# Performance work log

Measured on AMD Instinct MI355X. Metric: run time of the kernel, lower is better.

Reference implementation:

```python
import jax, jax.numpy as jnp
import numpy as np

DIMS = (8, 8, 16, 16)   # 4D lattice, prod = 16384 sites
ND = len(DIMS)
N_IN = 4
N_OUT = 4
NC = 3
KERNEL_SIZE = 2
DILATION = 0
INIT_W = 1.0

W_IN = 2 * N_IN + 1                                  # 9
T_W = 2 * (N_IN * (KERNEL_SIZE - 1) * ND) + 1        # 33


def cconj(w):
    # swap matrix indices (axes 3,4) and negate imaginary part (last axis)
    wT = jnp.swapaxes(w, 3, 4)
    return wT * jnp.array([1.0, -1.0], dtype=w.dtype)


def complex_einsum(pattern, a, b, conj_a=1, conj_b=1):
    aR, aI = a[..., 0], conj_a * a[..., 1]
    bR, bI = b[..., 0], conj_b * b[..., 1]
    cR = jnp.einsum(pattern, aR, bR) - jnp.einsum(pattern, aI, bI)
    cI = jnp.einsum(pattern, aR, bI) + jnp.einsum(pattern, aI, bR)
    return jnp.stack((cR, cI), axis=-1)


def shift(a, axis, orientation):
    # dim 1 is flattened lattice; unflatten, roll along lattice axis, re-flatten
    o_s = a.shape
    n_s = (o_s[0],) + DIMS + o_s[2:]
    return jnp.roll(a.reshape(n_s), orientation, axis=axis + 1).reshape(o_s)


def transport(u, w, axis):
    # positive-orientation gauge transport: U w(x+mu) U^dagger
    ws = shift(w, axis, -1)
    ua = u[:, :, axis]                                 # [b, x, nc, nc, 2]
    wt = complex_einsum('bxij,bxwjk->bxwik', ua, ws)
    wt = complex_einsum('bxwij,bxkj->bxwik', wt, ua, conj_b=-1)
    return wt


def setup_inputs() -> dict:
    key = jax.random.key(0)
    k1, k2 = jax.random.split(key)
    n_sites = int(np.prod(DIMS))
    x = jax.random.normal(k1, (1, n_sites, ND + N_IN, NC, NC, 2), dtype=jnp.float32)
    std = INIT_W * np.sqrt(1.0 / (W_IN * T_W))
    weight = jax.random.normal(k2, (N_OUT, W_IN, T_W), dtype=jnp.float32) * std
    return {"x": x, "weight": weight}


def reference(x, weight):
    u, w = x[:, :, :ND], x[:, :, ND:]
    transported = []
    for axis in range(ND):
        wt = w
        for d in range(1, KERNEL_SIZE):
            for _ in range(DILATION + 1):
                wt = transport(u, wt, axis)
            transported.append(wt)
    t_w = jnp.concatenate(transported, axis=2)          # [b, x, n_in*(K-1)*ND, nc, nc, 2]

    w_full = jnp.concatenate([w, cconj(w)], axis=2)
    t_w_full = jnp.concatenate([t_w, cconj(t_w)], axis=2)

    # unit element channel
    unit = jnp.stack((jnp.eye(NC, dtype=x.dtype), jnp.zeros((NC, NC), dtype=x.dtype)), axis=-1)
    b, n_sites = x.shape[0], x.shape[1]
    unit_t = jnp.broadcast_to(unit[None, None, None], (b, n_sites, 1, NC, NC, 2))
    w_full = jnp.concatenate([w_full, unit_t], axis=2)       # [b, x, 9, nc, nc, 2]
    t_w_full = jnp.concatenate([t_w_full, unit_t], axis=2)   # [b, x, 33, nc, nc, 2]

    # bilinear gauge-covariant products, then weight contraction
    ww = complex_einsum('bxvij,bxwjk->bxvwik', w_full, t_w_full)  # [b, x, 9, 33, nc, nc, 2]
    w_out = jnp.einsum('uvw,bxvwijc->bxuijc', weight, ww)         # [b, x, n_out, nc, nc, 2]

    return jnp.concatenate([u, w_out], axis=2)
```

## Files before the change

### kernel.cpp

```cpp
#include <hip/hip_runtime.h>
#include <stdint.h>


#define SPB 16
#define TPB 256
#define NSITES 16384
#define TS2_SITE 146
#define NWGT 1188

__device__ __forceinline__ float2 pk_fma(float2 a, float2 b, float2 c){
    return make_float2(fmaf(a.x, b.x, c.x), fmaf(a.y, b.y, c.y));
}
__device__ __forceinline__ float2 spl(float s){ return make_float2(s, s); }
__device__ __forceinline__ float2 pn(float s){ return make_float2(s, -s); }
__device__ __forceinline__ float2 np(float s){ return make_float2(-s, s); }
__device__ __forceinline__ float2 swp(float2 a){ return make_float2(a.y, a.x); }

__device__ __forceinline__ int neigh(int s, int a){
    if (a == 3) return (s & ~15)        | ((s + 1)    & 15);
    if (a == 2) return (s & ~(15 << 4)) | ((s + 16)   & (15 << 4));
    if (a == 1) return (s & ~(7 << 8))  | ((s + 256)  & (7 << 8));
    return              (s & ~(7 << 11))| ((s + 2048) & (7 << 11));
}

__global__ __launch_bounds__(TPB, 1)
void gcm_fused(const float* __restrict__ xp,
               const float* __restrict__ wgt,
               float* __restrict__ outp)
{
    __shared__ float2 lt[SPB * TS2_SITE];
    __shared__ float wsm[NWGT];
    const float2* x2 = (const float2*)xp;
    float2* o2 = (float2*)outp;

    const int tid = threadIdx.x;
    const int g   = tid & 3;
    const int u   = (tid >> 2) & 3;
    const int sl  = tid >> 4;
    const int s   = blockIdx.x * SPB + sl;

    for (int idx = tid; idx < NWGT; idx += TPB) wsm[idx] = wgt[idx];

    {
        const int a = u, i = g;
        float2 uc[9], wc[9];
        {
            const float2* up = x2 + (s * 8 + a) * 9;
            #pragma unroll
            for (int e = 0; e < 9; e++) uc[e] = up[e];
        }
        const int sn = neigh(s, a);
        {
            const float2* wp = x2 + (sn * 8 + 4 + i) * 9;
            #pragma unroll
            for (int e = 0; e < 9; e++) wc[e] = wp[e];
        }
        float2 t1[9];
        #pragma unroll
        for (int r = 0; r < 3; r++){
            #pragma unroll
            for (int k = 0; k < 3; k++){
                float2 acc = make_float2(0.f, 0.f);
                #pragma unroll
                for (int j = 0; j < 3; j++){
                    float2 a_ = uc[r*3+j], b_ = wc[j*3+k];
                    acc = pk_fma(spl(a_.x), b_, acc);
                    acc = pk_fma(np(a_.y), swp(b_), acc);
                }
                t1[r*3+k] = acc;
            }
        }
        float2* dst = &lt[sl * TS2_SITE + (a * 4 + i) * 9];
        #pragma unroll
        for (int r = 0; r < 3; r++){
            #pragma unroll
            for (int k = 0; k < 3; k++){
                float2 acc = make_float2(0.f, 0.f);
                #pragma unroll
                for (int j = 0; j < 3; j++){
                    float2 a_ = t1[r*3+j], b_ = uc[k*3+j];
                    acc = pk_fma(pn(a_.x), b_, acc);
                    acc = pk_fma(spl(a_.y), swp(b_), acc);
                }
                dst[r*3+k] = acc;
            }
        }
    }
    __syncthreads();

    if (g == 1){
        const float2* src = x2 + (s * 8 + u) * 9;
        float2* dst = o2 + (s * 8 + u) * 9;
        #pragma unroll
        for (int e = 0; e < 9; e++) dst[e] = src[e];
    }

    float2 wc[4][9];
    #pragma unroll
    for (int v = 0; v < 4; v++){
        const float2* wp = x2 + (s * 8 + 4 + v) * 9;
        #pragma unroll
        for (int e = 0; e < 9; e++) wc[v][e] = wp[e];
    }

    float2 cc[9];
    #pragma unroll
    for (int e = 0; e < 9; e++) cc[e] = make_float2(0.f, 0.f);

    const float* wu = wsm + u * 297;

    {
        #pragma unroll
        for (int v = 0; v < 4; v++){
            float c1 = (v == g) ? wu[v * 33 + 32]       : 0.f;
            float c2 = (v == g) ? wu[(4 + v) * 33 + 32] : 0.f;
            #pragma unroll
            for (int i = 0; i < 3; i++){
                #pragma unroll
                for (int j = 0; j < 3; j++){
                    const int e = i*3+j, eT = j*3+i;
                    cc[e] = pk_fma(spl(c1), wc[v][e],  cc[e]);
                    cc[e] = pk_fma(pn(c2),  wc[v][eT], cc[e]);
                }
            }
        }
        if (g == 0){
            float c8 = wu[8 * 33 + 32];
            cc[0].x += c8; cc[4].x += c8; cc[8].x += c8;
        }
    }

    const float2* tbase = &lt[sl * TS2_SITE];
    #pragma unroll
    for (int k = 0; k < 4; k++){
        const int w16 = g * 4 + k;
        float2 tc[9];
        {
            const float2* tp = tbase + w16 * 9;
            #pragma unroll
            for (int e = 0; e < 9; e++) tc[e] = tp[e];
        }

        {
            float cv[9];
            #pragma unroll
            for (int v = 0; v < 9; v++) cv[v] = wu[v * 33 + w16];
            #pragma unroll
            for (int i = 0; i < 3; i++){
                float2 nrow[3];
                #pragma unroll
                for (int j = 0; j < 3; j++){
                    const int e = i*3+j, eT = j*3+i;
                    float2 n = (i == j) ? make_float2(cv[8], 0.f) : make_float2(0.f, 0.f);
                    #pragma unroll
                    for (int v = 0; v < 4; v++){
                        n = pk_fma(spl(cv[v]),   wc[v][e],  n);
                        n = pk_fma(pn(cv[4+v]),  wc[v][eT], n);
                    }
                    nrow[j] = n;
                }
                #pragma unroll
                for (int kk = 0; kk < 3; kk++){
                    float2 acc = cc[i*3+kk];
                    #pragma unroll
                    for (int j = 0; j < 3; j++){
                        float2 b_ = tc[j*3+kk];
                        acc = pk_fma(spl(nrow[j].x), b_,      acc);
                        acc = pk_fma(np(nrow[j].y),  swp(b_), acc);
                    }
                    cc[i*3+kk] = acc;
                }
            }
        }

        {
            float cv[9];
            #pragma unroll
            for (int v = 0; v < 9; v++) cv[v] = wu[v * 33 + 16 + w16];
            #pragma unroll
            for (int i = 0; i < 3; i++){
                float2 nrow[3];
                #pragma unroll
                for (int j = 0; j < 3; j++){
                    const int e = i*3+j, eT = j*3+i;
                    float2 n = (i == j) ? make_float2(cv[8], 0.f) : make_float2(0.f, 0.f);
                    #pragma unroll
                    for (int v = 0; v < 4; v++){
                        n = pk_fma(spl(cv[v]),   wc[v][e],  n);
                        n = pk_fma(pn(cv[4+v]),  wc[v][eT], n);
                    }
                    nrow[j] = n;
                }
                #pragma unroll
                for (int kk = 0; kk < 3; kk++){
                    float2 acc = cc[i*3+kk];
                    #pragma unroll
                    for (int j = 0; j < 3; j++){
                        float2 b_ = tc[kk*3+j];
                        acc = pk_fma(pn(nrow[j].x),  b_,      acc);
                        acc = pk_fma(spl(nrow[j].y), swp(b_), acc);
                    }
                    cc[i*3+kk] = acc;
                }
            }
        }
    }

    #pragma unroll
    for (int e = 0; e < 9; e++){
        cc[e].x += __shfl_xor(cc[e].x, 1);
        cc[e].x += __shfl_xor(cc[e].x, 2);
        cc[e].y += __shfl_xor(cc[e].y, 1);
        cc[e].y += __shfl_xor(cc[e].y, 2);
    }
    if (g == 0){
        float2* dst = o2 + (s * 8 + 4 + u) * 9;
        #pragma unroll
        for (int e = 0; e < 9; e++) dst[e] = cc[e];
    }
}

extern "C" void kernel_launch(void* const* d_in, const int* in_sizes, int n_in,
                              void* d_out, int out_size, void* d_ws, size_t ws_size,
                              hipStream_t stream)
{
    const float* x = (const float*)d_in[0];
    const float* w = (const float*)d_in[1];
    float* out = (float*)d_out;
    dim3 grid(NSITES / SPB);
    dim3 block(TPB);
    hipLaunchKernelGGL(gcm_fused, grid, block, 0, stream, x, w, out);
}
```

Measured before the change: 88.93 us.

## Reassociate bilinear contraction: per-input weighted sums of transported fields

Each thread now owns one input channel g. It first accumulates two weighted linear combinations M1 and M2 of all 16 transported matrices (and their conjugates) from shared memory, then does just two 3x3 complex matmuls with w_g and its conjugate at the end. Before, each thread rebuilt weighted sums of all 4 w matrices for each of its own transported matrices and then did a matmul for each. The reordering cuts the 3x3 matmul count and drops the per-thread copy of all four w matrices, lowering register pressure. Launch bounds are raised to 2 blocks per SM to allow more occupancy. In exchange, each thread now reads all 16 transported matrices from LDS instead of 4, which raises LDS traffic.

```diff
diff --git a/kernel.cpp b/kernel.cpp
--- a/kernel.cpp
+++ b/kernel.cpp
@@ -23,7 +23,7 @@
     return              (s & ~(7 << 11))| ((s + 2048) & (7 << 11));
 }
 
-__global__ __launch_bounds__(TPB, 1)
+__global__ __launch_bounds__(TPB, 2)
 void gcm_fused(const float* __restrict__ xp,
                const float* __restrict__ wgt,
                float* __restrict__ outp)
@@ -95,114 +95,104 @@
         for (int e = 0; e < 9; e++) dst[e] = src[e];
     }
 
-    float2 wc[4][9];
-    #pragma unroll
-    for (int v = 0; v < 4; v++){
-        const float2* wp = x2 + (s * 8 + 4 + v) * 9;
-        #pragma unroll
-        for (int e = 0; e < 9; e++) wc[v][e] = wp[e];
-    }
-
-    float2 cc[9];
-    #pragma unroll
-    for (int e = 0; e < 9; e++) cc[e] = make_float2(0.f, 0.f);
-
-    const float* wu = wsm + u * 297;
-
+    float2 wg[9];
     {
-        #pragma unroll
-        for (int v = 0; v < 4; v++){
-            float c1 = (v == g) ? wu[v * 33 + 32]       : 0.f;
-            float c2 = (v == g) ? wu[(4 + v) * 33 + 32] : 0.f;
-            #pragma unroll
-            for (int i = 0; i < 3; i++){
-                #pragma unroll
-                for (int j = 0; j < 3; j++){
-                    const int e = i*3+j, eT = j*3+i;
-                    cc[e] = pk_fma(spl(c1), wc[v][e],  cc[e]);
-                    cc[e] = pk_fma(pn(c2),  wc[v][eT], cc[e]);
-                }
-            }
-        }
+        const float2* wp = x2 + (s * 8 + 4 + g) * 9;
+        #pragma unroll
+        for (int e = 0; e < 9; e++) wg[e] = wp[e];
+    }
+
+    float2 M1[9], M2[9], cc[9];
+    #pragma unroll
+    for (int e = 0; e < 9; e++){
+        M1[e] = make_float2(0.f, 0.f);
+        M2[e] = make_float2(0.f, 0.f);
+        cc[e] = make_float2(0.f, 0.f);
+    }
+
+    const float* wu  = wsm + u * 297;
+    const float* wuA = wu + g * 33;
+    const float* wuB = wu + (4 + g) * 33;
+    const float* wu8 = wu + 8 * 33;
+
+    const float2* tbase = &lt[sl * TS2_SITE];
+
+    #pragma unroll
+    for (int it = 0; it < 4; it++){
+        const int w16 = g * 4 + it;
+        const float2* tp = tbase + w16 * 9;
+        float2 tc[9];
+        #pragma unroll
+        for (int e = 0; e < 9; e++) tc[e] = tp[e];
+        float a1 = wuA[w16], b1 = wuA[16 + w16];
+        float a2 = wuB[w16], b2 = wuB[16 + w16];
+        float c8 = wu8[w16], d8 = wu8[16 + w16];
+        #pragma unroll
+        for (int i = 0; i < 3; i++){
+            #pragma unroll
+            for (int j = 0; j < 3; j++){
+                const int e = i*3+j, eT = j*3+i;
+                M1[e] = pk_fma(spl(a1), tc[e],  M1[e]);
+                M1[e] = pk_fma(pn(b1),  tc[eT], M1[e]);
+                M2[e] = pk_fma(spl(a2), tc[e],  M2[e]);
+                M2[e] = pk_fma(pn(b2),  tc[eT], M2[e]);
+                cc[e] = pk_fma(spl(c8), tc[e],  cc[e]);
+                cc[e] = pk_fma(pn(d8),  tc[eT], cc[e]);
+            }
+        }
+    }
+    #pragma unroll 4
+    for (int it = 0; it < 12; it++){
+        const int w16 = (g * 4 + 4 + it) & 15;
+        const float2* tp = tbase + w16 * 9;
+        float2 tc[9];
+        #pragma unroll
+        for (int e = 0; e < 9; e++) tc[e] = tp[e];
+        float a1 = wuA[w16], b1 = wuA[16 + w16];
+        float a2 = wuB[w16], b2 = wuB[16 + w16];
+        #pragma unroll
+        for (int i = 0; i < 3; i++){
+            #pragma unroll
+            for (int j = 0; j < 3; j++){
+                const int e = i*3+j, eT = j*3+i;
+                M1[e] = pk_fma(spl(a1), tc[e],  M1[e]);
+                M1[e] = pk_fma(pn(b1),  tc[eT], M1[e]);
+                M2[e] = pk_fma(spl(a2), tc[e],  M2[e]);
+                M2[e] = pk_fma(pn(b2),  tc[eT], M2[e]);
+            }
+        }
+    }
+
+    {
+        float c1 = wuA[32], c2 = wuB[32];
+        M1[0].x += c1; M1[4].x += c1; M1[8].x += c1;
+        M2[0].x += c2; M2[4].x += c2; M2[8].x += c2;
         if (g == 0){
-            float c8 = wu[8 * 33 + 32];
-            cc[0].x += c8; cc[4].x += c8; cc[8].x += c8;
-        }
-    }
-
-    const float2* tbase = &lt[sl * TS2_SITE];
-    #pragma unroll
-    for (int k = 0; k < 4; k++){
-        const int w16 = g * 4 + k;
-        float2 tc[9];
-        {
-            const float2* tp = tbase + w16 * 9;
-            #pragma unroll
-            for (int e = 0; e < 9; e++) tc[e] = tp[e];
-        }
-
-        {
-            float cv[9];
-            #pragma unroll
-            for (int v = 0; v < 9; v++) cv[v] = wu[v * 33 + w16];
-            #pragma unroll
-            for (int i = 0; i < 3; i++){
-                float2 nrow[3];
-                #pragma unroll
-                for (int j = 0; j < 3; j++){
-                    const int e = i*3+j, eT = j*3+i;
-                    float2 n = (i == j) ? make_float2(cv[8], 0.f) : make_float2(0.f, 0.f);
-                    #pragma unroll
-                    for (int v = 0; v < 4; v++){
-                        n = pk_fma(spl(cv[v]),   wc[v][e],  n);
-                        n = pk_fma(pn(cv[4+v]),  wc[v][eT], n);
-                    }
-                    nrow[j] = n;
-                }
-                #pragma unroll
-                for (int kk = 0; kk < 3; kk++){
-                    float2 acc = cc[i*3+kk];
-                    #pragma unroll
-                    for (int j = 0; j < 3; j++){
-                        float2 b_ = tc[j*3+kk];
-                        acc = pk_fma(spl(nrow[j].x), b_,      acc);
-                        acc = pk_fma(np(nrow[j].y),  swp(b_), acc);
-                    }
-                    cc[i*3+kk] = acc;
-                }
-            }
-        }
-
-        {
-            float cv[9];
-            #pragma unroll
-            for (int v = 0; v < 9; v++) cv[v] = wu[v * 33 + 16 + w16];
-            #pragma unroll
-            for (int i = 0; i < 3; i++){
-                float2 nrow[3];
-                #pragma unroll
-                for (int j = 0; j < 3; j++){
-                    const int e = i*3+j, eT = j*3+i;
-                    float2 n = (i == j) ? make_float2(cv[8], 0.f) : make_float2(0.f, 0.f);
-                    #pragma unroll
-                    for (int v = 0; v < 4; v++){
-                        n = pk_fma(spl(cv[v]),   wc[v][e],  n);
-                        n = pk_fma(pn(cv[4+v]),  wc[v][eT], n);
-                    }
-                    nrow[j] = n;
-                }
-                #pragma unroll
-                for (int kk = 0; kk < 3; kk++){
-                    float2 acc = cc[i*3+kk];
-                    #pragma unroll
-                    for (int j = 0; j < 3; j++){
-                        float2 b_ = tc[kk*3+j];
-                        acc = pk_fma(pn(nrow[j].x),  b_,      acc);
-                        acc = pk_fma(spl(nrow[j].y), swp(b_), acc);
-                    }
-                    cc[i*3+kk] = acc;
-                }
-            }
+            float e8 = wu8[32];
+            cc[0].x += e8; cc[4].x += e8; cc[8].x += e8;
+        }
+    }
+
+    #pragma unroll
+    for (int i = 0; i < 3; i++){
+        #pragma unroll
+        for (int k = 0; k < 3; k++){
+            float2 acc = cc[i*3+k];
+            #pragma unroll
+            for (int j = 0; j < 3; j++){
+                float2 a_ = wg[i*3+j];
+                float2 m  = M1[j*3+k];
+                acc = pk_fma(spl(a_.x), m,      acc);
+                acc = pk_fma(np(a_.y),  swp(m), acc);
+            }
+            #pragma unroll
+            for (int j = 0; j < 3; j++){
+                float2 b_ = wg[j*3+i];
+                float2 m  = M2[j*3+k];
+                acc = pk_fma(spl(b_.x), m,      acc);
+                acc = pk_fma(pn(b_.y),  swp(m), acc);
+            }
+            cc[i*3+k] = acc;
         }
     }
 
```

Measured after the change: 77.32 us. -13.1%, faster.
